# Performance work log

Measured on AMD Instinct MI355X. Metric: run time of the kernel, lower is better.

The kernel has to match this reference:

```python
import jax, jax.numpy as jnp
import numpy as np

NUM_HEADS = 12


def _rel_indices(H, W):
    # [N, N, 3] with channels (dx, dy, dx^2+dy^2), N = H*W
    indx = jnp.arange(W)[None, :] - jnp.arange(W)[:, None]          # [W, W]
    indx = jnp.tile(indx, (H, H))                                    # [N, N]
    indy = jnp.arange(H)[None, :] - jnp.arange(H)[:, None]          # [H, H]
    indy = jnp.repeat(jnp.repeat(indy, W, axis=0), W, axis=1)        # [N, N]
    indd = indx ** 2 + indy ** 2
    return jnp.stack([indx, indy, indd], axis=-1).astype(jnp.float32)


def setup_inputs() -> dict:
    key = jax.random.key(0)
    ks = jax.random.split(key, 8)
    B, N, C = 16, 576, 768
    std = 0.02
    return {
        "x": jax.random.normal(ks[0], (B, N, C), dtype=jnp.float32),
        "Wq": jax.random.normal(ks[1], (C, C), dtype=jnp.float32) * std,
        "Wk": jax.random.normal(ks[2], (C, C), dtype=jnp.float32) * std,
        "Wv": jax.random.normal(ks[3], (C, C), dtype=jnp.float32) * std,
        "Wproj": jax.random.normal(ks[4], (C, C), dtype=jnp.float32) * std,
        "bproj": jnp.zeros((C,), dtype=jnp.float32),
        "pos_w": jax.random.normal(ks[5], (3, NUM_HEADS), dtype=jnp.float32) * std,
        "pos_b": jnp.zeros((NUM_HEADS,), dtype=jnp.float32),
        "gating": jnp.ones((NUM_HEADS,), dtype=jnp.float32),
        "H": 24,
        "W": 24,
    }


def reference(x, Wq, Wk, Wv, Wproj, bproj, pos_w, pos_b, gating, H, W):
    B, N, C = x.shape
    h = gating.shape[0]
    d = C // h
    scale = d ** (-0.5)

    def heads(t):  # [B,N,C] -> [B,h,N,d]
        return t.reshape(B, N, h, d).transpose(0, 2, 1, 3)

    q = heads(x @ Wq)
    k = heads(x @ Wk)
    v = heads(x @ Wv)

    # content scores: [B,h,N,N]
    patch_score = jax.nn.softmax(jnp.einsum('bhnd,bhmd->bhnm', q, k) * scale, axis=-1)

    # positional scores: shared across batch, [h,N,N]
    rel = _rel_indices(H, W)                      # [N,N,3]
    pos_score = jnp.einsum('nmc,ch->hnm', rel, pos_w) + pos_b[:, None, None]
    pos_score = jax.nn.softmax(pos_score, axis=-1)

    gate = jax.nn.sigmoid(gating)[None, :, None, None]  # [1,h,1,1]
    attn = (1.0 - gate) * patch_score + gate * pos_score[None]
    attn = attn / jnp.sum(attn, axis=-1, keepdims=True)

    out = jnp.einsum('bhnm,bhmd->bhnd', attn, v)         # [B,h,N,d]
    out = out.transpose(0, 2, 1, 3).reshape(B, N, C)
    return out @ Wproj + bproj
```

## Files before the change

kernel.cpp:

```cpp
#include <hip/hip_runtime.h>
#include <math.h>

#define B_ 16
#define N_ 576
#define C_ 768
#define NH 12
#define D_ 64
#define GW 24
#define STR 68
#define QKV 2304
#define CSTR 136

typedef unsigned short u16;
typedef __bf16 bf16x8 __attribute__((ext_vector_type(8)));
typedef float f32x4 __attribute__((ext_vector_type(4)));

__device__ __forceinline__ u16 f2bf(float f) {
    unsigned u = __builtin_bit_cast(unsigned, f);
    unsigned r = (u + 0x7FFFu + ((u >> 16) & 1u)) >> 16;
    return (u16)r;
}
__device__ __forceinline__ float bf2f(u16 b) {
    unsigned u = ((unsigned)b) << 16;
    return __builtin_bit_cast(float, u);
}

__device__ __forceinline__ bf16x8 ldsF8u(const u16* p) {
    union { uint2 u[2]; bf16x8 v; } t;
    t.u[0] = *(const uint2*)p;
    t.u[1] = *(const uint2*)(p + 4);
    return t.v;
}
__device__ __forceinline__ bf16x8 ldsF8a(const u16* p) {
    union { uint4 u; bf16x8 v; } t;
    t.u = *(const uint4*)p;
    return t.v;
}

__device__ __forceinline__ void gload16(const u16* g, u16* l) {
    __builtin_amdgcn_global_load_lds(
        (const __attribute__((address_space(1))) void*)g,
        (__attribute__((address_space(3))) void*)l,
        16, 0, 0);
}

__global__ __launch_bounds__(256)
void prep_kernel(const float* __restrict__ x,
                 const float* __restrict__ w0, const float* __restrict__ w1,
                 const float* __restrict__ w2, const float* __restrict__ w3,
                 u16* __restrict__ xb, u16* __restrict__ wt_base)
{
    const int tid = threadIdx.x;
    if (blockIdx.z == 4) {
        const int flat = blockIdx.y * 24 + blockIdx.x;
#pragma unroll
        for (int it = 0; it < 12; ++it) {
            int idx = flat * 3072 + it * 256 + tid;
            float4 v = ((const float4*)x)[idx];
            u16 o[4] = {f2bf(v.x), f2bf(v.y), f2bf(v.z), f2bf(v.w)};
            *(uint2*)&xb[(size_t)idx * 4] = *(const uint2*)o;
        }
        return;
    }
    const float* srcs[4] = {w0, w1, w2, w3};
    const float* src = srcs[blockIdx.z];
    u16* dst = wt_base + (size_t)blockIdx.z * C_ * C_;
    __shared__ float t[32][33];
    const int bx = blockIdx.x * 32, by = blockIdx.y * 32;
    const int tx = tid & 31, ty = tid >> 5;
#pragma unroll
    for (int i = 0; i < 32; i += 8)
        t[ty + i][tx] = src[(size_t)(by + ty + i) * C_ + bx + tx];
    __syncthreads();
#pragma unroll
    for (int i = 0; i < 32; i += 8)
        dst[(size_t)(bx + ty + i) * C_ + by + tx] = f2bf(t[tx][ty + i]);
}

__global__ __launch_bounds__(256)
void mfma_gemm(const u16* __restrict__ A,
               const u16* __restrict__ BT,
               const float* __restrict__ bias,
               float* __restrict__ out,
               u16* __restrict__ outb,
               int ldo, int mode)
{
    const int K = C_;
    __shared__ __align__(16) u16 smem[128 * CSTR];
    u16* As = smem;
    u16* Bs = smem + 128 * 64;
    const int tid = threadIdx.x;
    const int wave = tid >> 6, lane = tid & 63;
    const int quad = lane >> 4, l16 = lane & 15;
    const int wy = wave >> 1, wx = wave & 1;
    const int tm = blockIdx.y * 128, tn = blockIdx.x * 128;

    const int lr = lane >> 3;
    const int sc = ((lane & 7) ^ lr) * 8;

    f32x4 acc[4][4];
#pragma unroll
    for (int i = 0; i < 4; ++i)
#pragma unroll
        for (int j = 0; j < 4; ++j)
            acc[i][j] = (f32x4){0.f, 0.f, 0.f, 0.f};

    for (int k0 = 0; k0 < K; k0 += 64) {
        __syncthreads();
#pragma unroll
        for (int t = 0; t < 4; ++t) {
            const int rg = wave * 32 + t * 8;
            gload16(A  + (size_t)(tm + rg + lr) * K + k0 + sc, &As[rg * 64]);
            gload16(BT + (size_t)(tn + rg + lr) * K + k0 + sc, &Bs[rg * 64]);
        }
        __syncthreads();

#pragma unroll
        for (int kh = 0; kh < 2; ++kh) {
            bf16x8 aA[4], bB[4];
#pragma unroll
            for (int i = 0; i < 4; ++i) {
                const int s = (kh * 4 + quad) ^ (l16 & 7);
                aA[i] = ldsF8a(&As[(wy * 64 + i * 16 + l16) * 64 + s * 8]);
            }
#pragma unroll
            for (int j = 0; j < 4; ++j) {
                const int s = (kh * 4 + quad) ^ (l16 & 7);
                bB[j] = ldsF8a(&Bs[(wx * 64 + j * 16 + l16) * 64 + s * 8]);
            }
#pragma unroll
            for (int i = 0; i < 4; ++i)
#pragma unroll
                for (int j = 0; j < 4; ++j)
                    acc[i][j] = __builtin_amdgcn_mfma_f32_16x16x32_bf16(bB[j], aA[i], acc[i][j], 0, 0, 0);
        }
    }

    if (mode == 0) {
#pragma unroll
        for (int i = 0; i < 4; ++i) {
            const int m = tm + wy * 64 + i * 16 + l16;
#pragma unroll
            for (int j = 0; j < 4; ++j) {
                const int c = tn + wx * 64 + j * 16 + quad * 4;
                float4 bv = *(const float4*)&bias[c];
                float4 o;
                o.x = acc[i][j][0] + bv.x;
                o.y = acc[i][j][1] + bv.y;
                o.z = acc[i][j][2] + bv.z;
                o.w = acc[i][j][3] + bv.w;
                *(float4*)&out[(size_t)m * ldo + c] = o;
            }
        }
    } else {
        const float scale = (tn < C_) ? 0.125f : 1.0f;
        __syncthreads();
#pragma unroll
        for (int i = 0; i < 4; ++i) {
            const int ml = wy * 64 + i * 16 + l16;
#pragma unroll
            for (int j = 0; j < 4; ++j) {
                const int cl = wx * 64 + j * 16 + quad * 4;
                u16 o[4];
#pragma unroll
                for (int r = 0; r < 4; ++r) o[r] = f2bf(acc[i][j][r] * scale);
                *(uint2*)&smem[ml * CSTR + cl] = *(const uint2*)o;
            }
        }
        __syncthreads();
#pragma unroll
        for (int p = 0; p < 2; ++p) {
            const int idx = p * 256 + tid;
            const int row = idx >> 2, qq = idx & 3;
            const u16* srcl = &smem[row * CSTR + qq * 32];
            u16* dstg = outb + (size_t)(tm + row) * ldo + tn + qq * 32;
#pragma unroll
            for (int t = 0; t < 4; ++t)
                *(uint4*)(dstg + t * 8) = *(const uint4*)(srcl + t * 8);
        }
    }
}

__global__ __launch_bounds__(256)
void tv_pos1_kernel(const u16* __restrict__ qkvb,
                    const float* __restrict__ pos_w,
                    u16* __restrict__ vtb,
                    float* __restrict__ T1)
{
    const int bh = blockIdx.y;
    const int b = bh / NH, h = bh % NH;
    const int tid = threadIdx.x;

    if (blockIdx.x < 9) {
        __shared__ u16 t[64 * 72];
        const int n0 = blockIdx.x * 64;
        const u16* src = qkvb + ((size_t)b * N_ + n0) * QKV + 2 * C_ + h * D_;
#pragma unroll
        for (int p = 0; p < 2; ++p) {
            int idx = p * 256 + tid;
            int r = idx >> 3, c = (idx & 7) << 3;
            *(uint4*)&t[r * 72 + c] = *(const uint4*)(src + (size_t)r * QKV + c);
        }
        __syncthreads();
        u16* dst = vtb + (size_t)bh * D_ * N_ + n0;
#pragma unroll
        for (int p = 0; p < 2; ++p) {
            int idx = p * 256 + tid;
            int dd = idx >> 3, n8 = (idx & 7) << 3;
            u16 o[8];
#pragma unroll
            for (int j = 0; j < 8; ++j) o[j] = t[(n8 + j) * 72 + dd];
            *(uint4*)(dst + (size_t)dd * N_ + n8) = *(const uint4*)o;
        }
        return;
    }

    __shared__ float ey[47];
    const float w1 = pos_w[NH + h], w2 = pos_w[2 * NH + h];
    if (tid < 47) {
        float dy = (float)(tid - 23);
        ey[tid] = __expf(w1 * dy + w2 * dy * dy);
    }
    __syncthreads();
    if (tid >= 192) return;
    const int mx = tid >> 3, c = (tid & 7) << 3;
    const u16* src = qkvb + (size_t)b * N_ * QKV + 2 * C_ + h * D_ + c;

#pragma unroll
    for (int np = 0; np < 3; ++np) {
        float acc[8][8];
#pragma unroll
        for (int q = 0; q < 8; ++q)
#pragma unroll
            for (int j = 0; j < 8; ++j) acc[q][j] = 0.f;
        for (int my = 0; my < GW; ++my) {
            union { uint4 u; u16 s[8]; } d;
            d.u = *(const uint4*)(src + (size_t)(my * GW + mx) * QKV);
            float vf[8];
#pragma unroll
            for (int j = 0; j < 8; ++j) vf[j] = bf2f(d.s[j]);
#pragma unroll
            for (int q = 0; q < 8; ++q) {
                float e = ey[my - (np * 8 + q) + 23];
#pragma unroll
                for (int j = 0; j < 8; ++j) acc[q][j] += e * vf[j];
            }
        }
#pragma unroll
        for (int q = 0; q < 8; ++q) {
            const int ny = np * 8 + q;
            float* dst = T1 + (((size_t)bh * GW + ny) * GW + mx) * D_ + c;
            *(float4*)dst       = *(float4*)&acc[q][0];
            *(float4*)(dst + 4) = *(float4*)&acc[q][4];
        }
    }
}

__global__ __launch_bounds__(256)
void pos_stage2_kernel(const float* __restrict__ T1,
                       const float* __restrict__ pos_w,
                       const float* __restrict__ gating,
                       u16* __restrict__ aob)
{
    const int bh = blockIdx.x;
    const int ny = blockIdx.y;
    const int b = bh / NH, h = bh % NH;
    const int tid = threadIdx.x;
    __shared__ float T1s[GW * D_];
    __shared__ float ex[47];
    __shared__ float SxA[GW];
    __shared__ float Sy;
    const float w0 = pos_w[h], w1 = pos_w[NH + h], w2 = pos_w[2 * NH + h];

    const float* tsrc = T1 + ((size_t)bh * GW + ny) * GW * D_;
#pragma unroll
    for (int i = 0; i < 2; ++i) {
        int idx = i * 256 + tid;
        if (idx < 384) ((float4*)T1s)[idx] = ((const float4*)tsrc)[idx];
    }
    if (tid < 47) {
        float dx = (float)(tid - 23);
        ex[tid] = __expf(w0 * dx + w2 * dx * dx);
    }
    if (tid == 192) {
        float s = 0.f;
        for (int my = 0; my < GW; ++my) {
            float dy = (float)(my - ny);
            s += __expf(w1 * dy + w2 * dy * dy);
        }
        Sy = s;
    }
    __syncthreads();
    if (tid < GW) {
        float s = 0.f;
        for (int mx = 0; mx < GW; ++mx) s += ex[mx - tid + 23];
        SxA[tid] = s;
    }
    __syncthreads();
    if (tid >= 192) return;
    const int nx = tid >> 3, c = (tid & 7) << 3;

    float acc[8];
#pragma unroll
    for (int j = 0; j < 8; ++j) acc[j] = 0.f;
    for (int mx = 0; mx < GW; ++mx) {
        float e = ex[mx - nx + 23];
        float4 t0 = *(float4*)&T1s[mx * D_ + c];
        float4 t1 = *(float4*)&T1s[mx * D_ + c + 4];
        acc[0] += e * t0.x; acc[1] += e * t0.y; acc[2] += e * t0.z; acc[3] += e * t0.w;
        acc[4] += e * t1.x; acc[5] += e * t1.y; acc[6] += e * t1.z; acc[7] += e * t1.w;
    }
    const float g = 1.f / (1.f + __expf(-gating[h]));
    const float sc = g / (SxA[nx] * Sy);
    const int n = ny * GW + nx;
    u16* dst = aob + ((size_t)b * N_ + n) * C_ + h * D_ + c;
    u16 cur[8];
    *(uint4*)cur = *(const uint4*)dst;
    u16 o[8];
#pragma unroll
    for (int j = 0; j < 8; ++j) o[j] = f2bf(bf2f(cur[j]) + sc * acc[j]);
    *(uint4*)dst = *(const uint4*)o;
}

__global__ __launch_bounds__(256)
void attn_kernel(const u16* __restrict__ qkvb,
                 const u16* __restrict__ vt,
                 const float* __restrict__ gating,
                 u16* __restrict__ ao)
{
    const int qt = blockIdx.x;
    const int bh = blockIdx.y;
    const int b = bh / NH, h = bh % NH;
    const int tid = threadIdx.x;
    const int wave = tid >> 6, lane = tid & 63;
    const int quad = lane >> 4, l16 = lane & 15;

    __shared__ u16 smem[3 * 64 * STR];
    u16* Kt = smem;
    u16* Vs = smem + 64 * STR;
    u16* Pb = smem + 2 * 64 * STR;

    const u16* qptr  = qkvb + ((size_t)b * N_ + qt * 64) * QKV + h * D_;
    const u16* kbase = qkvb + (size_t)b * N_ * QKV + C_ + h * D_;
    const u16* vbase = vt + (size_t)bh * D_ * N_;

    const int sr = tid >> 3;
    const int scol = (tid & 7) << 3;

#pragma unroll
    for (int p = 0; p < 2; ++p) {
        int r = p * 32 + sr;
        uint4 d = *(const uint4*)(qptr + (size_t)r * QKV + scol);
        *(uint2*)&Pb[r * STR + scol]     = make_uint2(d.x, d.y);
        *(uint2*)&Pb[r * STR + scol + 4] = make_uint2(d.z, d.w);
    }
    __syncthreads();

    const int arow = wave * 16 + l16;
    bf16x8 aq0 = ldsF8u(&Pb[arow * STR + quad * 8]);
    bf16x8 aq1 = ldsF8u(&Pb[arow * STR + 32 + quad * 8]);

    uint4 rk[2], rv[2];
    auto loadT = [&](int m0) {
#pragma unroll
        for (int p = 0; p < 2; ++p) {
            int r = p * 32 + sr;
            rk[p] = *(const uint4*)(kbase + (size_t)(m0 + r) * QKV + scol);
            rv[p] = *(const uint4*)(vbase + (size_t)r * N_ + m0 + scol);
        }
    };
    auto writeT = [&]() {
#pragma unroll
        for (int p = 0; p < 2; ++p) {
            int r = p * 32 + sr;
            *(uint2*)&Kt[r * STR + scol]     = make_uint2(rk[p].x, rk[p].y);
            *(uint2*)&Kt[r * STR + scol + 4] = make_uint2(rk[p].z, rk[p].w);
            *(uint2*)&Vs[r * STR + scol]     = make_uint2(rv[p].x, rv[p].y);
            *(uint2*)&Vs[r * STR + scol + 4] = make_uint2(rv[p].z, rv[p].w);
        }
    };

    loadT(0);

    f32x4 oc[4];
#pragma unroll
    for (int nt = 0; nt < 4; ++nt)
        oc[nt] = (f32x4){0.f, 0.f, 0.f, 0.f};
    float lrun[4] = {0.f, 0.f, 0.f, 0.f};

    for (int mt = 0; mt < 9; ++mt) {
        __syncthreads();
        writeT();
        __syncthreads();
        if (mt < 8) loadT((mt + 1) * 64);

        f32x4 s[4];
#pragma unroll
        for (int nt = 0; nt < 4; ++nt) {
            bf16x8 b0 = ldsF8u(&Kt[(nt * 16 + l16) * STR + quad * 8]);
            bf16x8 b1 = ldsF8u(&Kt[(nt * 16 + l16) * STR + 32 + quad * 8]);
            f32x4 z = (f32x4){0.f, 0.f, 0.f, 0.f};
            z = __builtin_amdgcn_mfma_f32_16x16x32_bf16(aq0, b0, z, 0, 0, 0);
            z = __builtin_amdgcn_mfma_f32_16x16x32_bf16(aq1, b1, z, 0, 0, 0);
            s[nt] = z;
        }

#pragma unroll
        for (int r = 0; r < 4; ++r) {
            const int prow = (wave * 16 + quad * 4 + r) * STR;
            float e0 = __expf(s[0][r]);
            float e1 = __expf(s[1][r]);
            float e2 = __expf(s[2][r]);
            float e3 = __expf(s[3][r]);
            Pb[prow +  0 + l16] = f2bf(e0);
            Pb[prow + 16 + l16] = f2bf(e1);
            Pb[prow + 32 + l16] = f2bf(e2);
            Pb[prow + 48 + l16] = f2bf(e3);
            lrun[r] += (e0 + e1) + (e2 + e3);
        }
        asm volatile("s_waitcnt lgkmcnt(0)" ::: "memory");

#pragma unroll
        for (int ks = 0; ks < 2; ++ks) {
            bf16x8 ap = ldsF8u(&Pb[arow * STR + ks * 32 + quad * 8]);
#pragma unroll
            for (int nt = 0; nt < 4; ++nt) {
                bf16x8 bv = ldsF8u(&Vs[(nt * 16 + l16) * STR + ks * 32 + quad * 8]);
                oc[nt] = __builtin_amdgcn_mfma_f32_16x16x32_bf16(ap, bv, oc[nt], 0, 0, 0);
            }
        }
    }

#pragma unroll
    for (int r = 0; r < 4; ++r) {
        lrun[r] += __shfl_xor(lrun[r], 1, 64);
        lrun[r] += __shfl_xor(lrun[r], 2, 64);
        lrun[r] += __shfl_xor(lrun[r], 4, 64);
        lrun[r] += __shfl_xor(lrun[r], 8, 64);
    }

    const float g = 1.f / (1.f + __expf(-gating[h]));
#pragma unroll
    for (int r = 0; r < 4; ++r) {
        const float sc = (1.f - g) / lrun[r];
        const int row = qt * 64 + wave * 16 + quad * 4 + r;
#pragma unroll
        for (int nt = 0; nt < 4; ++nt) {
            ao[((size_t)b * N_ + row) * C_ + h * D_ + nt * 16 + l16] =
                f2bf(oc[nt][r] * sc);
        }
    }
}

extern "C" void kernel_launch(void* const* d_in, const int* in_sizes, int n_in,
                              void* d_out, int out_size, void* d_ws, size_t ws_size,
                              hipStream_t stream)
{
    const float* x      = (const float*)d_in[0];
    const float* Wq     = (const float*)d_in[1];
    const float* Wk     = (const float*)d_in[2];
    const float* Wv     = (const float*)d_in[3];
    const float* Wproj  = (const float*)d_in[4];
    const float* bproj  = (const float*)d_in[5];
    const float* pos_w  = (const float*)d_in[6];
    const float* gating = (const float*)d_in[8];
    float* out = (float*)d_out;

    const size_t xe = (size_t)B_ * N_ * C_;
    const size_t we = (size_t)C_ * C_;
    const size_t qe = (size_t)B_ * N_ * QKV;
    u16* xb   = (u16*)d_ws;
    u16* wt   = xb + xe;
    u16* qkvb = wt + 4 * we;
    u16* vtb  = qkvb + qe;
    u16* aob  = vtb + xe;
    float* T1 = (float*)(aob + xe);
    size_t need = (size_t)(3 * xe + 4 * we + qe) * sizeof(u16)
                + (size_t)B_ * NH * GW * GW * D_ * sizeof(float);
    if (ws_size < need) return;

    prep_kernel<<<dim3(24, 24, 5), 256, 0, stream>>>(x, Wq, Wk, Wv, Wproj, xb, wt);

    mfma_gemm<<<dim3(18, 72), 256, 0, stream>>>(xb, wt, nullptr, nullptr,
                                                qkvb, QKV, 1);
    tv_pos1_kernel<<<dim3(10, B_ * NH), 256, 0, stream>>>(qkvb, pos_w, vtb, T1);
    attn_kernel<<<dim3(9, B_ * NH), 256, 0, stream>>>(qkvb, vtb, gating, aob);
    pos_stage2_kernel<<<dim3(B_ * NH, GW), 256, 0, stream>>>(T1, pos_w, gating, aob);
    mfma_gemm<<<dim3(6, 72), 256, 0, stream>>>(aob, wt + 3 * we, bproj, out,
                                               nullptr, C_, 0);
}
```

Measured before the change: 274.2 us.

## Halve GEMM M-tile and write MFMA results directly without LDS staging

Shrinks the GEMM block tile from 128x128 to 64x128, doubling the grid to improve occupancy and wave balance on the CUs. The MFMA operand order is swapped so the accumulator rows map to output rows, and the epilogue now writes scalar results straight to global memory instead of staging through shared memory. This removes epilogue barriers and LDS traffic, but lowers B-tile reuse and replaces vectorized stores with narrow per-element stores.

```diff
diff --git a/kernel.cpp b/kernel.cpp
--- a/kernel.cpp
+++ b/kernel.cpp
@@ -9,7 +9,6 @@
 #define GW 24
 #define STR 68
 #define QKV 2304
-#define CSTR 136
 
 typedef unsigned short u16;
 typedef __bf16 bf16x8 __attribute__((ext_vector_type(8)));
@@ -86,21 +85,20 @@
                int ldo, int mode)
 {
     const int K = C_;
-    __shared__ __align__(16) u16 smem[128 * CSTR];
-    u16* As = smem;
-    u16* Bs = smem + 128 * 64;
+    __shared__ __align__(16) u16 As[64 * 64];
+    __shared__ __align__(16) u16 Bs[128 * 64];
     const int tid = threadIdx.x;
     const int wave = tid >> 6, lane = tid & 63;
     const int quad = lane >> 4, l16 = lane & 15;
     const int wy = wave >> 1, wx = wave & 1;
-    const int tm = blockIdx.y * 128, tn = blockIdx.x * 128;
+    const int tm = blockIdx.y * 64, tn = blockIdx.x * 128;
 
     const int lr = lane >> 3;
     const int sc = ((lane & 7) ^ lr) * 8;
 
-    f32x4 acc[4][4];
-#pragma unroll
-    for (int i = 0; i < 4; ++i)
+    f32x4 acc[2][4];
+#pragma unroll
+    for (int i = 0; i < 2; ++i)
 #pragma unroll
         for (int j = 0; j < 4; ++j)
             acc[i][j] = (f32x4){0.f, 0.f, 0.f, 0.f};
@@ -108,75 +106,61 @@
     for (int k0 = 0; k0 < K; k0 += 64) {
         __syncthreads();
 #pragma unroll
+        for (int t = 0; t < 2; ++t) {
+            const int rg = wave * 16 + t * 8;
+            gload16(A + (size_t)(tm + rg + lr) * K + k0 + sc, &As[rg * 64]);
+        }
+#pragma unroll
         for (int t = 0; t < 4; ++t) {
             const int rg = wave * 32 + t * 8;
-            gload16(A  + (size_t)(tm + rg + lr) * K + k0 + sc, &As[rg * 64]);
             gload16(BT + (size_t)(tn + rg + lr) * K + k0 + sc, &Bs[rg * 64]);
         }
         __syncthreads();
 
 #pragma unroll
         for (int kh = 0; kh < 2; ++kh) {
-            bf16x8 aA[4], bB[4];
-#pragma unroll
-            for (int i = 0; i < 4; ++i) {
-                const int s = (kh * 4 + quad) ^ (l16 & 7);
-                aA[i] = ldsF8a(&As[(wy * 64 + i * 16 + l16) * 64 + s * 8]);
-            }
-#pragma unroll
-            for (int j = 0; j < 4; ++j) {
-                const int s = (kh * 4 + quad) ^ (l16 & 7);
+            const int s = (kh * 4 + quad) ^ (l16 & 7);
+            bf16x8 aA[2], bB[4];
+#pragma unroll
+            for (int i = 0; i < 2; ++i)
+                aA[i] = ldsF8a(&As[(wy * 32 + i * 16 + l16) * 64 + s * 8]);
+#pragma unroll
+            for (int j = 0; j < 4; ++j)
                 bB[j] = ldsF8a(&Bs[(wx * 64 + j * 16 + l16) * 64 + s * 8]);
-            }
-#pragma unroll
-            for (int i = 0; i < 4; ++i)
+#pragma unroll
+            for (int i = 0; i < 2; ++i)
 #pragma unroll
                 for (int j = 0; j < 4; ++j)
-                    acc[i][j] = __builtin_amdgcn_mfma_f32_16x16x32_bf16(bB[j], aA[i], acc[i][j], 0, 0, 0);
+                    acc[i][j] = __builtin_amdgcn_mfma_f32_16x16x32_bf16(aA[i], bB[j], acc[i][j], 0, 0, 0);
         }
     }
 
     if (mode == 0) {
 #pragma unroll
-        for (int i = 0; i < 4; ++i) {
-            const int m = tm + wy * 64 + i * 16 + l16;
-#pragma unroll
-            for (int j = 0; j < 4; ++j) {
-                const int c = tn + wx * 64 + j * 16 + quad * 4;
-                float4 bv = *(const float4*)&bias[c];
-                float4 o;
-                o.x = acc[i][j][0] + bv.x;
-                o.y = acc[i][j][1] + bv.y;
-                o.z = acc[i][j][2] + bv.z;
-                o.w = acc[i][j][3] + bv.w;
-                *(float4*)&out[(size_t)m * ldo + c] = o;
+        for (int i = 0; i < 2; ++i) {
+#pragma unroll
+            for (int r = 0; r < 4; ++r) {
+                const int m = tm + wy * 32 + i * 16 + quad * 4 + r;
+#pragma unroll
+                for (int j = 0; j < 4; ++j) {
+                    const int c = tn + wx * 64 + j * 16 + l16;
+                    out[(size_t)m * ldo + c] = acc[i][j][r] + bias[c];
+                }
             }
         }
     } else {
         const float scale = (tn < C_) ? 0.125f : 1.0f;
-        __syncthreads();
-#pragma unroll
-        for (int i = 0; i < 4; ++i) {
-            const int ml = wy * 64 + i * 16 + l16;
-#pragma unroll
-            for (int j = 0; j < 4; ++j) {
-                const int cl = wx * 64 + j * 16 + quad * 4;
-                u16 o[4];
-#pragma unroll
-                for (int r = 0; r < 4; ++r) o[r] = f2bf(acc[i][j][r] * scale);
-                *(uint2*)&smem[ml * CSTR + cl] = *(const uint2*)o;
+#pragma unroll
+        for (int i = 0; i < 2; ++i) {
+#pragma unroll
+            for (int r = 0; r < 4; ++r) {
+                const int m = tm + wy * 32 + i * 16 + quad * 4 + r;
+#pragma unroll
+                for (int j = 0; j < 4; ++j) {
+                    const int c = tn + wx * 64 + j * 16 + l16;
+                    outb[(size_t)m * ldo + c] = f2bf(acc[i][j][r] * scale);
+                }
             }
-        }
-        __syncthreads();
-#pragma unroll
-        for (int p = 0; p < 2; ++p) {
-            const int idx = p * 256 + tid;
-            const int row = idx >> 2, qq = idx & 3;
-            const u16* srcl = &smem[row * CSTR + qq * 32];
-            u16* dstg = outb + (size_t)(tm + row) * ldo + tn + qq * 32;
-#pragma unroll
-            for (int t = 0; t < 4; ++t)
-                *(uint4*)(dstg + t * 8) = *(const uint4*)(srcl + t * 8);
         }
     }
 }
@@ -481,11 +465,11 @@
 
     prep_kernel<<<dim3(24, 24, 5), 256, 0, stream>>>(x, Wq, Wk, Wv, Wproj, xb, wt);
 
-    mfma_gemm<<<dim3(18, 72), 256, 0, stream>>>(xb, wt, nullptr, nullptr,
-                                                qkvb, QKV, 1);
+    mfma_gemm<<<dim3(18, 144), 256, 0, stream>>>(xb, wt, nullptr, nullptr,
+                                                 qkvb, QKV, 1);
     tv_pos1_kernel<<<dim3(10, B_ * NH), 256, 0, stream>>>(qkvb, pos_w, vtb, T1);
     attn_kernel<<<dim3(9, B_ * NH), 256, 0, stream>>>(qkvb, vtb, gating, aob);
     pos_stage2_kernel<<<dim3(B_ * NH, GW), 256, 0, stream>>>(T1, pos_w, gating, aob);
-    mfma_gemm<<<dim3(6, 72), 256, 0, stream>>>(aob, wt + 3 * we, bproj, out,
-                                               nullptr, C_, 0);
-}
+    mfma_gemm<<<dim3(6, 144), 256, 0, stream>>>(aob, wt + 3 * we, bproj, out,
+                                                nullptr, C_, 0);
+}
```

Measured after the change: 261.0 us. 4.8% less time.
